# Kernel tuning notes

Measured on AMD Instinct MI355X. Metric: run time of the kernel, lower is better.

## Reference

```python
import jax, jax.numpy as jnp
import numpy as np


def conv(x, w, groups=1):
    # x: NCHW, w: OIHW, stride 1, SAME padding
    return jax.lax.conv_general_dilated(
        x, w, (1, 1), 'SAME', feature_group_count=groups,
        dimension_numbers=('NCHW', 'OIHW', 'NCHW'))


def bn(x, scale, shift):
    # eval-mode BatchNorm folded into per-channel affine
    return x * scale[None, :, None, None] + shift[None, :, None, None]


def ghost_expert(x, Wp, sp, bp, Wc, sc, bc, out_ch):
    # primary conv 3x3 (C_in -> init_ch) + BN + SiLU
    x1 = jax.nn.silu(bn(conv(x, Wp), sp, bp))
    # cheap depthwise 3x3 (groups = init_ch) + BN + SiLU
    x2 = jax.nn.silu(bn(conv(x1, Wc, groups=x1.shape[1]), sc, bc))
    return jnp.concatenate([x1, x2], axis=1)[:, :out_ch]


def setup_inputs() -> dict:
    key = jax.random.key(0)
    ks = jax.random.split(key, 20)
    B, Cin, Cout, H, W = 8, 256, 256, 64, 64
    E, red, init_ch, new_ch = 4, 32, 128, 128
    f = lambda k, shape, s=0.05: jax.random.normal(k, shape, jnp.float32) * s
    g = lambda k, shape: jax.random.uniform(k, shape, jnp.float32, 0.5, 1.5)
    inp = dict(
        x=jax.random.normal(ks[0], (B, Cin, H, W), jnp.float32),
        # router: conv3x3 Cin->red, BN, SiLU, conv1x1 red->E, BN
        Wr1=f(ks[1], (red, Cin, 3, 3)), sr1=g(ks[2], (red,)), br1=f(ks[3], (red,), 0.1),
        Wr2=f(ks[4], (E, red, 1, 1)), sr2=g(ks[5], (E,)), br2=f(ks[6], (E,), 0.1),
        # E ghost experts (stacked on leading expert axis)
        We_p=f(ks[7], (E, init_ch, Cin, 3, 3)), se_p=g(ks[8], (E, init_ch)), be_p=f(ks[9], (E, init_ch), 0.1),
        We_c=f(ks[10], (E, new_ch, 1, 3, 3)), se_c=g(ks[11], (E, new_ch)), be_c=f(ks[12], (E, new_ch), 0.1),
        # shared ghost expert
        Ws_p=f(ks[13], (init_ch, Cin, 3, 3)), ss_p=g(ks[14], (init_ch,)), bs_p=f(ks[15], (init_ch,), 0.1),
        Ws_c=f(ks[16], (new_ch, 1, 3, 3)), ss_c=g(ks[17], (new_ch,)), bs_c=f(ks[18], (new_ch,), 0.1),
        top_k=2,
    )
    return inp


def reference(x, Wr1, sr1, br1, Wr2, sr2, br2,
              We_p, se_p, be_p, We_c, se_c, be_c,
              Ws_p, ss_p, bs_p, Ws_c, ss_c, bs_c, top_k):
    B, Cin, H, W = x.shape
    E = Wr2.shape[0]
    Cout = 256
    pool_scale = 4
    # ---- EfficientSpatialRouter (eval mode: no noise) ----
    xd = x.reshape(B, Cin, H // pool_scale, pool_scale, W // pool_scale, pool_scale).mean((3, 5))
    h = jax.nn.silu(bn(conv(xd, Wr1), sr1, br1))
    logits = bn(conv(h, Wr2), sr2, br2)           # [B, E, H/4, W/4]
    global_logits = logits.mean(axis=(2, 3))      # [B, E]
    weights = jax.nn.softmax(global_logits, axis=1)
    topk_vals, topk_idx = jax.lax.top_k(weights, top_k)
    topk_vals = topk_vals / (topk_vals.sum(axis=1, keepdims=True) + 1e-6)
    # ---- dense all-expert compute + weighted combine ----
    run = lambda Wp, sp, bp, Wc, sc, bc: ghost_expert(x, Wp, sp, bp, Wc, sc, bc, Cout)
    expert_outs = jax.vmap(run)(We_p, se_p, be_p, We_c, se_c, be_c)  # [E,B,Cout,H,W]
    w_full = (topk_vals[:, :, None] * jax.nn.one_hot(topk_idx, E, dtype=x.dtype)).sum(1)  # [B,E]
    combined = jnp.einsum('be,ebchw->bchw', w_full, expert_outs)
    # ---- shared expert for stability ----
    shared = ghost_expert(x, Ws_p, ss_p, bs_p, Ws_c, ss_c, bs_c, Cout)
    return combined + shared
```

## Files before the change

kernel.cpp:

```cpp
#include <hip/hip_runtime.h>
#include <hip/hip_bf16.h>

constexpr int BATCH = 8;
constexpr int CIN   = 256;
constexpr int HH    = 64;
constexpr int WW    = 64;
constexpr int NPIX  = HH * WW;
constexpr int ICH   = 128;

constexpr size_t OFF_XD    = 0;
constexpr size_t OFF_HMEAN = 524288;
constexpr size_t OFF_WFULL = 524544;
constexpr size_t OFF_SLOT  = 524608;
constexpr size_t OFF_WTB   = 524672;
constexpr size_t OFF_XBP   = OFF_WTB + 737280;
constexpr size_t OFF_X1B   = OFF_XBP + 4460544;

typedef __bf16  bf16x8 __attribute__((ext_vector_type(8)));
typedef float   f32x4  __attribute__((ext_vector_type(4)));

__device__ __forceinline__ float silu_f(float v) { return v / (1.f + __expf(-v)); }

__device__ __forceinline__ unsigned short f2bf(float f) {
    return __builtin_bit_cast(unsigned short, __float2bfloat16(f));
}
__device__ __forceinline__ float bf2f(unsigned short u) {
    return __builtin_bit_cast(float, (unsigned)u << 16);
}
__device__ __forceinline__ bf16x8 ld_frag(const ushort* p) {
    uint4 v = *(const uint4*)p;
    return __builtin_bit_cast(bf16x8, v);
}
__device__ __forceinline__ void gload16(const ushort* g, ushort* l) {
    __builtin_amdgcn_global_load_lds(
        (const __attribute__((address_space(1))) void*)g,
        (__attribute__((address_space(3))) void*)l, 16, 0, 0);
}

__global__ void k_avgpool(const float* __restrict__ x, float* __restrict__ xd)
{
    int t = blockIdx.x * 256 + threadIdx.x;
    int jb = t & 3, i = (t >> 2) & 15, c = (t >> 6) & 255, b = t >> 14;
    const float* src = x + ((size_t)(b * CIN + c) * HH + i * 4) * WW + jb * 16;
    float s0 = 0.f, s1 = 0.f, s2 = 0.f, s3 = 0.f;
#pragma unroll
    for (int r = 0; r < 4; ++r) {
        const float4* p = (const float4*)(src + r * WW);
        float4 a = p[0], b4 = p[1], c4 = p[2], d4 = p[3];
        s0 += a.x + a.y + a.z + a.w;
        s1 += b4.x + b4.y + b4.z + b4.w;
        s2 += c4.x + c4.y + c4.z + c4.w;
        s3 += d4.x + d4.y + d4.z + d4.w;
    }
    float4 o;
    o.x = s0 * 0.0625f; o.y = s1 * 0.0625f; o.z = s2 * 0.0625f; o.w = s3 * 0.0625f;
    *(float4*)(xd + ((size_t)(b * CIN + c) * 16 + i) * 16 + jb * 4) = o;
}

__global__ __launch_bounds__(256) void k_xprep(const float* __restrict__ x,
                                               ushort* __restrict__ xbp)
{
    int b = blockIdx.x >> 6, row = blockIdx.x & 63;
    __shared__ ushort tile[64 * 258];
    int tid = threadIdx.x;
    const float* src = x + ((size_t)b * CIN * HH + row) * WW;
    for (int k = tid; k < 256 * 64; k += 256) {
        int cin = k >> 6, col = k & 63;
        tile[col * 258 + cin] = f2bf(src[(size_t)cin * NPIX + col]);
    }
    __syncthreads();
    ushort* dst = xbp + ((size_t)(b * 66 + row + 1) * 66 + 1) * 256;
    for (int k = tid; k < 64 * 128; k += 256) {
        int col = k >> 7, cp = (k & 127) * 2;
        unsigned u0 = tile[col * 258 + cp];
        unsigned u1 = tile[col * 258 + cp + 1];
        *(unsigned*)(dst + (size_t)col * 256 + cp) = u0 | (u1 << 16);
    }
}

__global__ __launch_bounds__(256) void k_router_conv(
    const float* __restrict__ xd, const float* __restrict__ Wr1,
    const float* __restrict__ sr1, const float* __restrict__ br1,
    float* __restrict__ hmean)
{
    int b = blockIdx.x >> 5, r = blockIdx.x & 31;
    __shared__ float wl[9 * 256];
    __shared__ float red[256];
    int tid = threadIdx.x;
    for (int k = tid; k < 2304; k += 256) {
        int cin = k / 9, tap = k % 9;
        wl[tap * 256 + cin] = Wr1[r * 2304 + k];
    }
    __syncthreads();
    const float* xb = xd + (size_t)b * CIN * 256;
    int i = tid >> 4, j = tid & 15;
    float acc = 0.f;
#pragma unroll
    for (int kh = 0; kh < 3; ++kh) {
        int ii = i + kh - 1;
        bool oki = (unsigned)ii < 16u;
        int iis = oki ? ii : 0;
#pragma unroll
        for (int kw = 0; kw < 3; ++kw) {
            int jj = j + kw - 1;
            bool ok = oki && ((unsigned)jj < 16u);
            int off = iis * 16 + (((unsigned)jj < 16u) ? jj : 0);
            const float* wt = wl + (kh * 3 + kw) * 256;
            float t = 0.f;
#pragma unroll 8
            for (int cin = 0; cin < 256; ++cin)
                t = fmaf(wt[cin], xb[cin * 256 + off], t);
            if (ok) acc += t;
        }
    }
    float h = silu_f(acc * sr1[r] + br1[r]);
    red[tid] = h;
    __syncthreads();
    for (int st = 128; st > 0; st >>= 1) {
        if (tid < st) red[tid] += red[tid + st];
        __syncthreads();
    }
    if (tid == 0) hmean[b * 32 + r] = red[0] * (1.f / 256.f);
}

__global__ void k_router_final(const float* __restrict__ hmean,
                               const float* __restrict__ Wr2, const float* __restrict__ sr2,
                               const float* __restrict__ br2, const int* __restrict__ topk_p,
                               float* __restrict__ wfull, int* __restrict__ slot)
{
    __shared__ float lg[8][4];
    __shared__ float wf[8][5];
    int tid = threadIdx.x;
    if (tid < 32) {
        int b = tid >> 2, e = tid & 3;
        float a = 0.f;
        for (int r = 0; r < 32; ++r) a += Wr2[e * 32 + r] * hmean[b * 32 + r];
        lg[b][e] = a * sr2[e] + br2[e];
    }
    __syncthreads();
    if (tid < 8) {
        int b = tid;
        float l0 = lg[b][0], l1 = lg[b][1], l2 = lg[b][2], l3 = lg[b][3];
        float mx = fmaxf(fmaxf(l0, l1), fmaxf(l2, l3));
        float e0 = __expf(l0 - mx), e1 = __expf(l1 - mx), e2 = __expf(l2 - mx), e3 = __expf(l3 - mx);
        float sum = e0 + e1 + e2 + e3;
        float w[4] = { e0 / sum, e1 / sum, e2 / sum, e3 / sum };
        int k = topk_p[0];
        if (k > 4) k = 4;
        bool taken[4] = { false, false, false, false };
        float tv[4]; int ti[4]; float tsum = 0.f;
        for (int t = 0; t < k; ++t) {
            float best = -1e30f; int bi = 0;
            for (int e = 0; e < 4; ++e)
                if (!taken[e] && w[e] > best) { best = w[e]; bi = e; }
            taken[bi] = true; tv[t] = best; ti[t] = bi; tsum += best;
        }
        float inv = 1.f / (tsum + 1e-6f);
        float o[4] = { 0.f, 0.f, 0.f, 0.f };
        for (int t = 0; t < k; ++t) o[ti[t]] = tv[t] * inv;
        for (int e = 0; e < 4; ++e) { wf[b][e] = o[e]; wfull[b * 5 + e] = o[e]; }
        wf[b][4] = 1.f; wfull[b * 5 + 4] = 1.f;
    }
    __syncthreads();
    if (tid == 0) {
        int cnt = 0;
        for (int s = 0; s < 5; ++s)
            for (int b = 0; b < 8; ++b)
                slot[s * 8 + b] = (wf[b][s] != 0.f) ? (cnt++) : -1;
    }
}

__global__ void k_wprep16(const float* __restrict__ We_p, const float* __restrict__ Ws_p,
                          ushort* __restrict__ wtb)
{
    int t = blockIdx.x * 256 + threadIdx.x;
    int k5  = t & 31;
    int oc  = (t >> 5) & 63;
    int tap = (t >> 11) % 9;
    int blk = t / 18432;
    int chunk = blk & 7;
    int h     = (blk >> 3) & 1;
    int s     = blk >> 4;
    int cin   = chunk * 32 + k5;
    int ocg   = h * 64 + oc;
    float v = (s < 4) ? We_p[((size_t)(s * 128 + ocg) * 256 + cin) * 9 + tap]
                      : Ws_p[((size_t)ocg * 256 + cin) * 9 + tap];
    wtb[t] = f2bf(v);
}

__global__ __launch_bounds__(256, 3) void k_primary_mfma(
    const ushort* __restrict__ xbp, const ushort* __restrict__ wtb,
    const float* __restrict__ se_p, const float* __restrict__ be_p,
    const float* __restrict__ ss_p, const float* __restrict__ bs_p,
    const int* __restrict__ slot, ushort* __restrict__ x1b)
{
    int pass = blockIdx.y;
    int sl = slot[pass];
    if (sl < 0) return;
    int s = pass >> 3, b = pass & 7;
    int och = blockIdx.x >> 4;
    int tile = blockIdx.x & 15;
    int row0 = (tile >> 2) * 16, col0 = (tile & 3) * 16;

    __shared__ ushort xlds[2][1344 * 8];

    int tid = threadIdx.x;
    int wv = tid >> 6, lane = tid & 63;
    int ks = lane >> 4, c = lane & 15;

    const ushort* xb_b = xbp + (size_t)b * 66 * 66 * 256;

    int goff[6];
#pragma unroll
    for (int it = 0; it < 5; ++it) {
        int k = it * 256 + tid;
        int r = k / 72, rem = k % 72, ks2 = rem / 18, c2 = rem % 18;
        goff[it] = ((row0 + r) * 66 + (col0 + c2)) * 256 + ks2 * 8;
    }
    {
        int k = 1280 + lane;
        int r = k / 72, rem = k % 72, ks2 = rem / 18, c2 = rem % 18;
        goff[5] = ((row0 + r) * 66 + (col0 + c2)) * 256 + ks2 * 8;
    }
    int lds_us = wv * 512;

    f32x4 acc[4][4];
#pragma unroll
    for (int m = 0; m < 4; ++m)
#pragma unroll
        for (int n = 0; n < 4; ++n) acc[m][n] = (f32x4){0.f, 0.f, 0.f, 0.f};

    const ushort* wslab = wtb + (size_t)(s * 2 + och) * (8 * 18432);
    int Sb = 4 * wv * 72 + ks * 18 + c;

    {
        const ushort* src = xb_b;
#pragma unroll
        for (int it = 0; it < 5; ++it)
            gload16(src + goff[it], &xlds[0][(size_t)(it * 2048 + lds_us)]);
        if (wv == 0) gload16(src + goff[5], &xlds[0][1280 * 8]);
    }
    __syncthreads();

    int cur = 0;
    for (int ch = 0; ch < 8; ++ch) {
        if (ch < 7) {
            const ushort* src = xb_b + (ch + 1) * 32;
#pragma unroll
            for (int it = 0; it < 5; ++it)
                gload16(src + goff[it], &xlds[cur ^ 1][(size_t)(it * 2048 + lds_us)]);
            if (wv == 0) gload16(src + goff[5], &xlds[cur ^ 1][1280 * 8]);
        }
        const ushort* wsrc = wslab + ch * 18432;
        const ushort* xl = &xlds[cur][0];
#pragma unroll
        for (int kh = 0; kh < 3; ++kh) {
#pragma unroll
            for (int kw = 0; kw < 3; ++kw) {
                int tap = kh * 3 + kw;
                bf16x8 afr[4];
#pragma unroll
                for (int m = 0; m < 4; ++m)
                    afr[m] = ld_frag(wsrc + ((size_t)(tap * 64 + m * 16 + c) * 4 + ks) * 8);
#pragma unroll
                for (int n = 0; n < 4; ++n) {
                    bf16x8 bfr = ld_frag(xl + (size_t)(Sb + (n + kh) * 72 + kw) * 8);
#pragma unroll
                    for (int m = 0; m < 4; ++m)
                        acc[m][n] = __builtin_amdgcn_mfma_f32_16x16x32_bf16(
                            afr[m], bfr, acc[m][n], 0, 0, 0);
                }
            }
        }
        __syncthreads();
        cur ^= 1;
    }

    const float* scale = (s < 4) ? (se_p + s * ICH) : ss_p;
    const float* shift = (s < 4) ? (be_p + s * ICH) : bs_p;
    ushort* outp = x1b + (size_t)sl * (ICH * NPIX);
    int colg = col0 + c;
#pragma unroll
    for (int m = 0; m < 4; ++m) {
#pragma unroll
        for (int n = 0; n < 4; ++n) {
            int rowg = row0 + 4 * wv + n;
#pragma unroll
            for (int j = 0; j < 4; ++j) {
                int oc = och * 64 + m * 16 + ks * 4 + j;
                float v = acc[m][n][j] * scale[oc] + shift[oc];
                outp[(size_t)oc * NPIX + rowg * 64 + colg] = f2bf(silu_f(v));
            }
        }
    }
}

__global__ __launch_bounds__(256) void k_cheap(
    const ushort* __restrict__ x1b, const float* __restrict__ We_c,
    const float* __restrict__ se_c, const float* __restrict__ be_c,
    const float* __restrict__ Ws_c, const float* __restrict__ ss_c,
    const float* __restrict__ bs_c, const float* __restrict__ wfull,
    const int* __restrict__ slot, float* __restrict__ out)
{
    int blk = blockIdx.x;
    int b = blk >> 7, c = blk & 127;
    __shared__ float img[66][66];
    int tid = threadIdx.x;
    for (int k = tid; k < 66 * 66; k += 256) ((float*)img)[k] = 0.f;
    float o1[16], o2[16];
#pragma unroll
    for (int t = 0; t < 16; ++t) { o1[t] = 0.f; o2[t] = 0.f; }
    __syncthreads();

    for (int s = 0; s < 5; ++s) {
        int sl = slot[s * 8 + b];
        if (sl < 0) continue;
        float wgt = (s < 4) ? wfull[b * 5 + s] : 1.0f;
        const ushort* src = x1b + ((size_t)sl * ICH + c) * NPIX;
        for (int k = tid; k < NPIX / 2; k += 256) {
            int i = k >> 5, jc = (k & 31) * 2;
            unsigned u = *(const unsigned*)(src + i * 64 + jc);
            img[1 + i][1 + jc] = bf2f((unsigned short)(u & 0xFFFFu));
            img[1 + i][2 + jc] = bf2f((unsigned short)(u >> 16));
        }
        float wc[9], sc, sh;
        if (s < 4) {
            const float* wp = We_c + (size_t)(s * ICH + c) * 9;
#pragma unroll
            for (int t = 0; t < 9; ++t) wc[t] = wp[t];
            sc = se_c[s * ICH + c]; sh = be_c[s * ICH + c];
        } else {
            const float* wp = Ws_c + (size_t)c * 9;
#pragma unroll
            for (int t = 0; t < 9; ++t) wc[t] = wp[t];
            sc = ss_c[c]; sh = bs_c[c];
        }
        __syncthreads();
#pragma unroll
        for (int t = 0; t < 16; ++t) {
            int p = tid + t * 256;
            int i = p >> 6, j = p & 63;
            float center = img[1 + i][1 + j];
            float d = 0.f;
#pragma unroll
            for (int kh = 0; kh < 3; ++kh)
#pragma unroll
                for (int kw = 0; kw < 3; ++kw)
                    d = fmaf(wc[kh * 3 + kw], img[i + kh][j + kw], d);
            float v = d * sc + sh;
            o1[t] += wgt * center;
            o2[t] += wgt * silu_f(v);
        }
        __syncthreads();
    }

    float* out1 = out + ((size_t)(b * 256) + c) * NPIX;
    float* out2 = out + ((size_t)(b * 256) + 128 + c) * NPIX;
#pragma unroll
    for (int t = 0; t < 16; ++t) {
        int p = tid + t * 256;
        out1[p] = o1[t];
        out2[p] = o2[t];
    }
}

extern "C" void kernel_launch(void* const* d_in, const int* in_sizes, int n_in,
                              void* d_out, int out_size, void* d_ws, size_t ws_size,
                              hipStream_t stream)
{
    const float* x    = (const float*)d_in[0];
    const float* Wr1  = (const float*)d_in[1];
    const float* sr1  = (const float*)d_in[2];
    const float* br1  = (const float*)d_in[3];
    const float* Wr2  = (const float*)d_in[4];
    const float* sr2  = (const float*)d_in[5];
    const float* br2  = (const float*)d_in[6];
    const float* We_p = (const float*)d_in[7];
    const float* se_p = (const float*)d_in[8];
    const float* be_p = (const float*)d_in[9];
    const float* We_c = (const float*)d_in[10];
    const float* se_c = (const float*)d_in[11];
    const float* be_c = (const float*)d_in[12];
    const float* Ws_p = (const float*)d_in[13];
    const float* ss_p = (const float*)d_in[14];
    const float* bs_p = (const float*)d_in[15];
    const float* Ws_c = (const float*)d_in[16];
    const float* ss_c = (const float*)d_in[17];
    const float* bs_c = (const float*)d_in[18];
    const int*  topk  = (const int*)d_in[19];
    float* out = (float*)d_out;
    float* ws  = (float*)d_ws;

    float*  xd    = ws + OFF_XD;
    float*  hmean = ws + OFF_HMEAN;
    float*  wfull = ws + OFF_WFULL;
    int*    slot  = (int*)(ws + OFF_SLOT);
    ushort* wtb   = (ushort*)(ws + OFF_WTB);
    ushort* xbp   = (ushort*)(ws + OFF_XBP);
    ushort* x1b   = (ushort*)(ws + OFF_X1B);

    hipMemsetAsync(xbp, 0, (size_t)8 * 66 * 66 * 256 * sizeof(ushort), stream);
    k_avgpool<<<512, 256, 0, stream>>>(x, xd);
    k_xprep<<<512, 256, 0, stream>>>(x, xbp);
    k_wprep16<<<5760, 256, 0, stream>>>(We_p, Ws_p, wtb);
    k_router_conv<<<256, 256, 0, stream>>>(xd, Wr1, sr1, br1, hmean);
    k_router_final<<<1, 64, 0, stream>>>(hmean, Wr2, sr2, br2, topk, wfull, slot);
    k_primary_mfma<<<dim3(32, 40), 256, 0, stream>>>(xbp, wtb, se_p, be_p, ss_p, bs_p, slot, x1b);
    k_cheap<<<1024, 256, 0, stream>>>(x1b, We_c, se_c, be_c, Ws_c, ss_c, bs_c, wfull, slot, out);
}
```

Baseline: 365.0 us.

## Stage primary-conv weights in LDS and batch all active expert images in cheap kernel

The primary MFMA kernel now double-buffers the per-chunk weight slab into shared memory together with the input tile, so A fragments are read from LDS rather than global memory. Launch bounds drop to one block per SM to allow for the larger LDS footprint. The cheap depthwise kernel collects the up to three active expert slots first, loads all their images into a 3-deep LDS buffer with wider 8-byte loads, and then computes without per-expert barriers. The cost is much higher LDS use and lower occupancy in both kernels.

Result: faster. 301.9 us (-17.3%).

```diff
diff --git a/kernel.cpp b/kernel.cpp
--- a/kernel.cpp
+++ b/kernel.cpp
@@ -188,7 +188,7 @@
     wtb[t] = f2bf(v);
 }
 
-__global__ __launch_bounds__(256, 3) void k_primary_mfma(
+__global__ __launch_bounds__(256, 1) void k_primary_mfma(
     const ushort* __restrict__ xbp, const ushort* __restrict__ wtb,
     const float* __restrict__ se_p, const float* __restrict__ be_p,
     const float* __restrict__ ss_p, const float* __restrict__ bs_p,
@@ -202,6 +202,7 @@
     int tile = blockIdx.x & 15;
     int row0 = (tile >> 2) * 16, col0 = (tile & 3) * 16;
 
+    __shared__ ushort wlds[2][2304 * 8];
     __shared__ ushort xlds[2][1344 * 8];
 
     int tid = threadIdx.x;
@@ -209,6 +210,7 @@
     int ks = lane >> 4, c = lane & 15;
 
     const ushort* xb_b = xbp + (size_t)b * 66 * 66 * 256;
+    const ushort* wslab = wtb + (size_t)(s * 2 + och) * (8 * 18432);
 
     int goff[6];
 #pragma unroll
@@ -230,28 +232,28 @@
 #pragma unroll
         for (int n = 0; n < 4; ++n) acc[m][n] = (f32x4){0.f, 0.f, 0.f, 0.f};
 
-    const ushort* wslab = wtb + (size_t)(s * 2 + och) * (8 * 18432);
     int Sb = 4 * wv * 72 + ks * 18 + c;
 
-    {
-        const ushort* src = xb_b;
+    auto stage = [&](int ch, int buf) {
+        const ushort* wsrc = wslab + ch * 18432;
+#pragma unroll
+        for (int it = 0; it < 9; ++it)
+            gload16(wsrc + (size_t)(it * 256 + tid) * 8,
+                    &wlds[buf][(size_t)(it * 2048 + lds_us)]);
+        const ushort* xsrc = xb_b + ch * 32;
 #pragma unroll
         for (int it = 0; it < 5; ++it)
-            gload16(src + goff[it], &xlds[0][(size_t)(it * 2048 + lds_us)]);
-        if (wv == 0) gload16(src + goff[5], &xlds[0][1280 * 8]);
-    }
+            gload16(xsrc + goff[it], &xlds[buf][(size_t)(it * 2048 + lds_us)]);
+        if (wv == 0) gload16(xsrc + goff[5], &xlds[buf][1280 * 8]);
+    };
+
+    stage(0, 0);
     __syncthreads();
 
     int cur = 0;
     for (int ch = 0; ch < 8; ++ch) {
-        if (ch < 7) {
-            const ushort* src = xb_b + (ch + 1) * 32;
-#pragma unroll
-            for (int it = 0; it < 5; ++it)
-                gload16(src + goff[it], &xlds[cur ^ 1][(size_t)(it * 2048 + lds_us)]);
-            if (wv == 0) gload16(src + goff[5], &xlds[cur ^ 1][1280 * 8]);
-        }
-        const ushort* wsrc = wslab + ch * 18432;
+        if (ch < 7) stage(ch + 1, cur ^ 1);
+        const ushort* wl = &wlds[cur][0];
         const ushort* xl = &xlds[cur][0];
 #pragma unroll
         for (int kh = 0; kh < 3; ++kh) {
@@ -261,7 +263,7 @@
                 bf16x8 afr[4];
 #pragma unroll
                 for (int m = 0; m < 4; ++m)
-                    afr[m] = ld_frag(wsrc + ((size_t)(tap * 64 + m * 16 + c) * 4 + ks) * 8);
+                    afr[m] = ld_frag(wl + ((size_t)(tap * 64 + m * 16 + c) * 4 + ks) * 8);
 #pragma unroll
                 for (int n = 0; n < 4; ++n) {
                     bf16x8 bfr = ld_frag(xl + (size_t)(Sb + (n + kh) * 72 + kw) * 8);
@@ -304,54 +306,73 @@
 {
     int blk = blockIdx.x;
     int b = blk >> 7, c = blk & 127;
-    __shared__ float img[66][66];
+    __shared__ float img[3][66][66];
     int tid = threadIdx.x;
-    for (int k = tid; k < 66 * 66; k += 256) ((float*)img)[k] = 0.f;
-    float o1[16], o2[16];
-#pragma unroll
-    for (int t = 0; t < 16; ++t) { o1[t] = 0.f; o2[t] = 0.f; }
-    __syncthreads();
-
+
+    int nact = 0;
+    int sls[3], sidx[3];
+    float wgts[3];
     for (int s = 0; s < 5; ++s) {
         int sl = slot[s * 8 + b];
         if (sl < 0) continue;
-        float wgt = (s < 4) ? wfull[b * 5 + s] : 1.0f;
-        const ushort* src = x1b + ((size_t)sl * ICH + c) * NPIX;
-        for (int k = tid; k < NPIX / 2; k += 256) {
-            int i = k >> 5, jc = (k & 31) * 2;
-            unsigned u = *(const unsigned*)(src + i * 64 + jc);
-            img[1 + i][1 + jc] = bf2f((unsigned short)(u & 0xFFFFu));
-            img[1 + i][2 + jc] = bf2f((unsigned short)(u >> 16));
-        }
-        float wc[9], sc, sh;
-        if (s < 4) {
-            const float* wp = We_c + (size_t)(s * ICH + c) * 9;
-#pragma unroll
-            for (int t = 0; t < 9; ++t) wc[t] = wp[t];
-            sc = se_c[s * ICH + c]; sh = be_c[s * ICH + c];
-        } else {
-            const float* wp = Ws_c + (size_t)c * 9;
-#pragma unroll
-            for (int t = 0; t < 9; ++t) wc[t] = wp[t];
-            sc = ss_c[c]; sh = bs_c[c];
-        }
-        __syncthreads();
-#pragma unroll
-        for (int t = 0; t < 16; ++t) {
-            int p = tid + t * 256;
-            int i = p >> 6, j = p & 63;
-            float center = img[1 + i][1 + j];
-            float d = 0.f;
-#pragma unroll
-            for (int kh = 0; kh < 3; ++kh)
-#pragma unroll
-                for (int kw = 0; kw < 3; ++kw)
-                    d = fmaf(wc[kh * 3 + kw], img[i + kh][j + kw], d);
-            float v = d * sc + sh;
-            o1[t] += wgt * center;
-            o2[t] += wgt * silu_f(v);
-        }
-        __syncthreads();
+        sls[nact] = sl; sidx[nact] = s;
+        wgts[nact] = (s < 4) ? wfull[b * 5 + s] : 1.0f;
+        ++nact;
+    }
+
+    for (int k = tid; k < 3 * 66 * 66; k += 256) ((float*)img)[k] = 0.f;
+    __syncthreads();
+
+#pragma unroll
+    for (int a = 0; a < 3; ++a) {
+        if (a < nact) {
+            const ushort* src = x1b + ((size_t)sls[a] * ICH + c) * NPIX;
+            for (int k = tid; k < 1024; k += 256) {
+                int i = k >> 4, jc = (k & 15) * 4;
+                uint2 u = *(const uint2*)(src + i * 64 + jc);
+                img[a][1 + i][1 + jc] = bf2f((unsigned short)(u.x & 0xFFFFu));
+                img[a][1 + i][2 + jc] = bf2f((unsigned short)(u.x >> 16));
+                img[a][1 + i][3 + jc] = bf2f((unsigned short)(u.y & 0xFFFFu));
+                img[a][1 + i][4 + jc] = bf2f((unsigned short)(u.y >> 16));
+            }
+        }
+    }
+    __syncthreads();
+
+    float o1[16], o2[16];
+#pragma unroll
+    for (int t = 0; t < 16; ++t) { o1[t] = 0.f; o2[t] = 0.f; }
+
+#pragma unroll
+    for (int a = 0; a < 3; ++a) {
+        if (a < nact) {
+            int s = sidx[a];
+            const float* wp = (s < 4) ? (We_c + (size_t)(s * ICH + c) * 9)
+                                      : (Ws_c + (size_t)c * 9);
+            float wc0 = wp[0], wc1 = wp[1], wc2 = wp[2], wc3 = wp[3], wc4 = wp[4],
+                  wc5 = wp[5], wc6 = wp[6], wc7 = wp[7], wc8 = wp[8];
+            float sc = (s < 4) ? se_c[s * ICH + c] : ss_c[c];
+            float sh = (s < 4) ? be_c[s * ICH + c] : bs_c[c];
+            float wgt = wgts[a];
+#pragma unroll
+            for (int t = 0; t < 16; ++t) {
+                int p = tid + t * 256;
+                int i = p >> 6, j = p & 63;
+                float center = img[a][1 + i][1 + j];
+                float d = wc0 * img[a][i][j];
+                d = fmaf(wc1, img[a][i][j + 1], d);
+                d = fmaf(wc2, img[a][i][j + 2], d);
+                d = fmaf(wc3, img[a][i + 1][j], d);
+                d = fmaf(wc4, center, d);
+                d = fmaf(wc5, img[a][i + 1][j + 2], d);
+                d = fmaf(wc6, img[a][i + 2][j], d);
+                d = fmaf(wc7, img[a][i + 2][j + 1], d);
+                d = fmaf(wc8, img[a][i + 2][j + 2], d);
+                float v = d * sc + sh;
+                o1[t] += wgt * center;
+                o2[t] += wgt * silu_f(v);
+            }
+        }
     }
 
     float* out1 = out + ((size_t)(b * 256) + c) * NPIX;
```
